# Optimization experiments

Measured on AMD Instinct MI355X. Metric: run time of the kernel, lower is better.

Reference implementation:

```python
import jax, jax.numpy as jnp
import numpy as np

DIM = 192
HEADS = 6
G = 16          # window size (ds_flag=0 dense attention)
B = 1
H_SZ = 256
W_SZ = 256
POS_DIM = 12    # (dim//4)//4
HIDDEN = 768    # 4*dim


def _ln(x, g, b, eps=1e-5):
    m = jnp.mean(x, -1, keepdims=True)
    v = jnp.var(x, -1, keepdims=True)
    return (x - m) / jnp.sqrt(v + eps) * g + b


def setup_inputs() -> dict:
    key = jax.random.key(0)
    ks = jax.random.split(key, 8)
    s = 0.05
    return {
        "x": jax.random.normal(ks[0], (B, H_SZ * W_SZ, DIM), jnp.float32),
        "gamma1": jnp.ones((DIM,), jnp.float32),
        "beta1": jnp.zeros((DIM,), jnp.float32),
        "qkv_w": jax.random.normal(ks[1], (DIM, 3 * DIM), jnp.float32) * s,
        "qkv_b": jnp.zeros((3 * DIM,), jnp.float32),
        "proj_w": jax.random.normal(ks[2], (DIM, DIM), jnp.float32) * s,
        "proj_b": jnp.zeros((DIM,), jnp.float32),
        "pos_proj_w": jax.random.normal(ks[3], (2, POS_DIM), jnp.float32) * s,
        "pos_proj_b": jnp.zeros((POS_DIM,), jnp.float32),
        "ln1_g": jnp.ones((POS_DIM,), jnp.float32),
        "ln1_b": jnp.zeros((POS_DIM,), jnp.float32),
        "pos1_w": jax.random.normal(ks[4], (POS_DIM, POS_DIM), jnp.float32) * s,
        "pos1_b": jnp.zeros((POS_DIM,), jnp.float32),
        "ln2_g": jnp.ones((POS_DIM,), jnp.float32),
        "ln2_b": jnp.zeros((POS_DIM,), jnp.float32),
        "pos2_w": jax.random.normal(ks[5], (POS_DIM, POS_DIM), jnp.float32) * s,
        "pos2_b": jnp.zeros((POS_DIM,), jnp.float32),
        "ln3_g": jnp.ones((POS_DIM,), jnp.float32),
        "ln3_b": jnp.zeros((POS_DIM,), jnp.float32),
        "pos3_w": jax.random.normal(ks[6], (POS_DIM, HEADS), jnp.float32) * s,
        "pos3_b": jnp.zeros((HEADS,), jnp.float32),
        "gamma2": jnp.ones((DIM,), jnp.float32),
        "beta2": jnp.zeros((DIM,), jnp.float32),
        "fc1_w": jax.random.normal(ks[7], (DIM, HIDDEN), jnp.float32) * s,
        "fc1_b": jnp.zeros((HIDDEN,), jnp.float32),
        "fc2_w": jax.random.normal(jax.random.fold_in(key, 9), (HIDDEN, DIM), jnp.float32) * s,
        "fc2_b": jnp.zeros((DIM,), jnp.float32),
        "H": H_SZ,
        "W": W_SZ,
    }


def reference(x, gamma1, beta1, qkv_w, qkv_b, proj_w, proj_b,
              pos_proj_w, pos_proj_b, ln1_g, ln1_b, pos1_w, pos1_b,
              ln2_g, ln2_b, pos2_w, pos2_b, ln3_g, ln3_b, pos3_w, pos3_b,
              gamma2, beta2, fc1_w, fc1_b, fc2_w, fc2_b, H, W):
    Bx, L, C = x.shape
    h = HEADS
    d = C // h
    N = G * G
    shortcut = x
    xn = _ln(x, gamma1, beta1)
    # window partition (H, W divisible by G -> no padding, attn_mask=None)
    xw = xn.reshape(Bx, H // G, G, W // G, G, C).transpose(0, 1, 3, 2, 4, 5)
    xw = xw.reshape(-1, N, C)                       # [B_, N, C]
    B_ = xw.shape[0]
    qkv = (xw @ qkv_w + qkv_b).reshape(B_, N, 3, h, d)
    q = qkv[:, :, 0].transpose(0, 2, 1, 3) * (d ** -0.5)   # [B_, h, N, d]
    k = qkv[:, :, 1].transpose(0, 2, 1, 3)
    v = qkv[:, :, 2].transpose(0, 2, 1, 3)
    attn = jnp.einsum('bhnd,bhmd->bhnm', q, k)      # [B_, h, N, N]
    # dynamic relative position bias (DynamicPosBias MLP + gather)
    r = jnp.arange(1 - G, G)
    biases = jnp.stack(jnp.meshgrid(r, r, indexing='ij')).reshape(2, -1).T.astype(x.dtype)  # [(2G-1)^2, 2]
    p = biases @ pos_proj_w + pos_proj_b
    p = jax.nn.relu(_ln(p, ln1_g, ln1_b)) @ pos1_w + pos1_b
    p = jax.nn.relu(_ln(p, ln2_g, ln2_b)) @ pos2_w + pos2_b
    p = jax.nn.relu(_ln(p, ln3_g, ln3_b)) @ pos3_w + pos3_b  # [(2G-1)^2, heads]
    c = jnp.stack(jnp.meshgrid(jnp.arange(G), jnp.arange(G), indexing='ij')).reshape(2, -1)
    rel = c[:, :, None] - c[:, None, :]             # [2, N, N]
    idx = (rel[0] + G - 1) * (2 * G - 1) + (rel[1] + G - 1)  # [N, N]
    attn = attn + p[idx].transpose(2, 0, 1)[None]   # add [1, h, N, N] bias
    attn = jax.nn.softmax(attn, axis=-1)
    out = jnp.einsum('bhnm,bhmd->bhnd', attn, v).transpose(0, 2, 1, 3).reshape(B_, N, C)
    out = out @ proj_w + proj_b
    # window reverse
    out = out.reshape(Bx, H // G, W // G, G, G, C).transpose(0, 1, 3, 2, 4, 5).reshape(Bx, L, C)
    x = shortcut + out
    y = _ln(x, gamma2, beta2)
    y = jax.nn.gelu(y @ fc1_w + fc1_b, approximate=False) @ fc2_w + fc2_b
    return x + y
```

## Files before the change

### kernel.cpp

```cpp
#include <hip/hip_runtime.h>
#include <hip/hip_bf16.h>

#define DIM 192
#define HEADS 6
#define QKV_N 576
#define HIDDEN 768
#define M_ROWS 65536

typedef unsigned short ushortT;
typedef __attribute__((ext_vector_type(8))) short short8v;
typedef __attribute__((ext_vector_type(4))) float f32x4;
typedef __attribute__((ext_vector_type(4))) unsigned int u32x4;

#define QSCALE_L2E 0.2550348649f
#define LOG2E 1.4426950408889634f

__device__ __forceinline__ float bf2f(ushortT u) {
    union { unsigned int i; float f; } c; c.i = ((unsigned int)u) << 16; return c.f;
}
__device__ __forceinline__ ushortT f2bf(float f) {
    union { float f; unsigned int i; } c; c.f = f;
    unsigned int i = c.i;
    return (ushortT)((i + 0x7fffu + ((i >> 16) & 1u)) >> 16);
}

#define GLOBAL_LOAD_LDS16(gp, lp) \
    __builtin_amdgcn_global_load_lds((const __attribute__((address_space(1))) void*)(gp), \
                                     (__attribute__((address_space(3))) void*)(lp), 16, 0, 0)

__device__ __forceinline__ void ln_relu_mm12(const float* in, const float* g, const float* b,
                                             const float* w, const float* bb, float* out, int nout) {
    float m = 0.f;
#pragma unroll
    for (int j = 0; j < 12; ++j) m += in[j];
    m *= (1.0f / 12.0f);
    float v = 0.f;
#pragma unroll
    for (int j = 0; j < 12; ++j) { float d = in[j] - m; v += d * d; }
    v *= (1.0f / 12.0f);
    float r = rsqrtf(v + 1e-5f);
    float t[12];
#pragma unroll
    for (int j = 0; j < 12; ++j) t[j] = fmaxf((in[j] - m) * r * g[j] + b[j], 0.0f);
    for (int j2 = 0; j2 < nout; ++j2) {
        float s = bb[j2];
#pragma unroll
        for (int j = 0; j < 12; ++j) s = fmaf(t[j], w[j * nout + j2], s);
        out[j2] = s;
    }
}

__global__ __launch_bounds__(256) void prep_kernel(
        const float* __restrict__ qkv_w, const float* __restrict__ proj_w,
        const float* __restrict__ fc1_w, const float* __restrict__ fc2_w,
        ushortT* __restrict__ qkv_wt, ushortT* __restrict__ proj_wt,
        ushortT* __restrict__ fc1_wt, ushortT* __restrict__ fc2_wt,
        const float* __restrict__ pw, const float* __restrict__ pb,
        const float* __restrict__ g1, const float* __restrict__ b1,
        const float* __restrict__ w1, const float* __restrict__ bb1,
        const float* __restrict__ g2, const float* __restrict__ b2,
        const float* __restrict__ w2, const float* __restrict__ bb2,
        const float* __restrict__ g3, const float* __restrict__ b3,
        const float* __restrict__ w3, const float* __restrict__ bb3,
        float* __restrict__ BTf) {
    __shared__ float tile[32][33];
    int blk = blockIdx.x;
    int t = threadIdx.x;
    if (blk < 432) {
        const float* W; ushortT* Wt; int K, N, bx, by;
        if (blk < 108)      { W = qkv_w;  Wt = qkv_wt;  K = 192; N = 576; bx = blk % 18;        by = blk / 18; }
        else if (blk < 144) { int r = blk - 108; W = proj_w; Wt = proj_wt; K = 192; N = 192; bx = r % 6;  by = r / 6; }
        else if (blk < 288) { int r = blk - 144; W = fc1_w;  Wt = fc1_wt;  K = 192; N = 768; bx = r % 24; by = r / 24; }
        else                { int r = blk - 288; W = fc2_w;  Wt = fc2_wt;  K = 768; N = 192; bx = r % 6;  by = r / 6; }
        int tx = t & 31, ty = t >> 5;
        int bX = bx * 32, bY = by * 32;
#pragma unroll
        for (int i = 0; i < 32; i += 8)
            tile[ty + i][tx] = W[(size_t)(bY + ty + i) * N + bX + tx];
        __syncthreads();
#pragma unroll
        for (int i = 0; i < 32; i += 8)
            Wt[(size_t)(bX + ty + i) * K + bY + tx] = f2bf(tile[tx][ty + i]);
    } else {
        int blk2 = blk - 432;
        int h = blk2 >> 8, q = blk2 & 255, kv = t;
        float di = (float)((q >> 4) - (kv >> 4));
        float dj = (float)((q & 15) - (kv & 15));
        float a[12], hh[12];
#pragma unroll
        for (int j = 0; j < 12; ++j) a[j] = di * pw[j] + dj * pw[12 + j] + pb[j];
        ln_relu_mm12(a, g1, b1, w1, bb1, hh, 12);
        ln_relu_mm12(hh, g2, b2, w2, bb2, a, 12);
        float m = 0.f;
#pragma unroll
        for (int j = 0; j < 12; ++j) m += a[j];
        m *= (1.0f / 12.0f);
        float v = 0.f;
#pragma unroll
        for (int j = 0; j < 12; ++j) { float d = a[j] - m; v += d * d; }
        v *= (1.0f / 12.0f);
        float r = rsqrtf(v + 1e-5f);
        float s = bb3[h];
#pragma unroll
        for (int j = 0; j < 12; ++j)
            s = fmaf(fmaxf((a[j] - m) * r * g3[j] + b3[j], 0.0f), w3[j * 6 + h], s);
        int wid = q >> 6, mf = (q >> 4) & 3, l4 = (q >> 2) & 3, rr = q & 3;
        int kc = kv >> 5, cc = kv & 31;
        int cf = (cc >> 4) & 1, l15 = cc & 15;
        int lane = l4 * 16 + l15;
        size_t off = ((size_t)((h * 8 + kc) * 32 + wid * 8 + mf * 2 + cf)) * 256 + lane * 4 + rr;
        BTf[off] = s * LOG2E;
    }
}

__global__ __launch_bounds__(256) void ln_kernel(const float* __restrict__ x,
                                                 const float* __restrict__ g,
                                                 const float* __restrict__ b,
                                                 ushortT* __restrict__ out) {
    int lane = threadIdx.x & 63;
    size_t row = (size_t)blockIdx.x * 4 + (threadIdx.x >> 6);
    const float* xr = x + row * DIM;
    float v0 = xr[lane], v1 = xr[lane + 64], v2 = xr[lane + 128];
    float s = v0 + v1 + v2;
    float ss = v0 * v0 + v1 * v1 + v2 * v2;
#pragma unroll
    for (int off = 32; off > 0; off >>= 1) {
        s += __shfl_xor(s, off);
        ss += __shfl_xor(ss, off);
    }
    float mean = s * (1.0f / DIM);
    float rstd = rsqrtf(ss * (1.0f / DIM) - mean * mean + 1e-5f);
    ushortT* o = out + row * DIM;
    o[lane]       = f2bf((v0 - mean) * rstd * g[lane]       + b[lane]);
    o[lane + 64]  = f2bf((v1 - mean) * rstd * g[lane + 64]  + b[lane + 64]);
    o[lane + 128] = f2bf((v2 - mean) * rstd * g[lane + 128] + b[lane + 128]);
}

template <int MODE, int NY, int KK>
__global__ __launch_bounds__(256) void mfma_gemm(const ushortT* __restrict__ A,
                                                 const ushortT* __restrict__ Wt,
                                                 const float* __restrict__ bias,
                                                 const float* __restrict__ resid,
                                                 void* __restrict__ outp,
                                                 int N) {
    __shared__ ushortT As[2][128 * 64];
    __shared__ ushortT Bs[2][64 * 64];
    const int NT = KK / 64;
    int tid = threadIdx.x;
    int lane = tid & 63, wid = tid >> 6;
    int l15 = lane & 15, l4 = lane >> 4;
    int wr = wid >> 1, wc = wid & 1;
    int p = blockIdx.x;
    int cpx = gridDim.x >> 3;
    int logical = (p & 7) * cpx + (p >> 3);
    int bx = logical / NY;
    int by = logical - bx * NY;
    int bm = bx * 128, bn = by * 64;

    f32x4 acc[4][2];
#pragma unroll
    for (int mf = 0; mf < 4; ++mf)
#pragma unroll
        for (int nf = 0; nf < 2; ++nf)
#pragma unroll
            for (int r = 0; r < 4; ++r) acc[mf][nf][r] = 0.f;

    int srow = tid >> 3;
    int schunk = (tid & 7) ^ (srow & 7);
    const ushortT* agp = A + (size_t)(bm + srow) * KK + schunk * 8;
    const ushortT* bgp = Wt + (size_t)(bn + srow) * KK + schunk * 8;

    auto STAGE = [&](int buf, int t) {
        int k0 = t * 64;
#pragma unroll
        for (int i = 0; i < 4; ++i)
            GLOBAL_LOAD_LDS16(agp + (size_t)i * 32 * KK + k0, &As[buf][i * 2048 + wid * 512]);
#pragma unroll
        for (int i = 0; i < 2; ++i)
            GLOBAL_LOAD_LDS16(bgp + (size_t)i * 32 * KK + k0, &Bs[buf][i * 2048 + wid * 512]);
    };

    STAGE(0, 0);
    for (int t = 0; t < NT; ++t) {
        int cur = t & 1;
        if (t + 1 < NT) {
            STAGE(cur ^ 1, t + 1);
            asm volatile("s_waitcnt vmcnt(6)" ::: "memory");
        } else {
            asm volatile("s_waitcnt vmcnt(0)" ::: "memory");
        }
        __builtin_amdgcn_s_barrier();
        const ushortT* Asc = As[cur];
        const ushortT* Bsc = Bs[cur];
#pragma unroll
        for (int ks = 0; ks < 2; ++ks) {
            short8v af[4], bf[2];
#pragma unroll
            for (int mf = 0; mf < 4; ++mf) {
                int row = wr * 64 + mf * 16 + l15;
                af[mf] = *(const short8v*)&Asc[row * 64 + (((ks * 4 + l4) ^ (l15 & 7)) << 3)];
            }
#pragma unroll
            for (int nf = 0; nf < 2; ++nf) {
                int row = wc * 32 + nf * 16 + l15;
                bf[nf] = *(const short8v*)&Bsc[row * 64 + (((ks * 4 + l4) ^ (l15 & 7)) << 3)];
            }
#pragma unroll
            for (int mf = 0; mf < 4; ++mf)
#pragma unroll
                for (int nf = 0; nf < 2; ++nf)
                    acc[mf][nf] = __builtin_amdgcn_mfma_f32_16x16x32_bf16(af[mf], bf[nf], acc[mf][nf], 0, 0, 0);
        }
        __builtin_amdgcn_s_barrier();
    }
#pragma unroll
    for (int mf = 0; mf < 4; ++mf) {
        size_t row = (size_t)bm + wr * 64 + mf * 16 + l4 * 4;
#pragma unroll
        for (int nf = 0; nf < 2; ++nf) {
            int col = bn + wc * 32 + nf * 16 + l15;
            float bv = bias[col];
#pragma unroll
            for (int r = 0; r < 4; ++r) {
                size_t off = (row + r) * (size_t)N + col;
                float v = acc[mf][nf][r] + bv;
                if (MODE == 0) {
                    if (col < 192) v *= QSCALE_L2E;
                    ((ushortT*)outp)[off] = f2bf(v);
                } else if (MODE == 1) {
                    float x3 = v * v * v;
                    float z = fmaf(x3, -0.1029537917f, v * -2.302205077f);
                    float e = exp2f(z);
                    v = v * __builtin_amdgcn_rcpf(1.0f + e);
                    ((ushortT*)outp)[off] = f2bf(v);
                } else if (MODE == 2) {
                    ((float*)outp)[off] = resid[off] + v;
                } else {
                    ((float*)outp)[off] += v;
                }
            }
        }
    }
}

__global__ __launch_bounds__(256) void attn_mfma_kernel(const ushortT* __restrict__ qkv,
                                                        const float* __restrict__ BTf,
                                                        ushortT* __restrict__ O) {
    __shared__ ushortT Vt[32][264];
    __shared__ unsigned int Ps[4][64][20];
    int wh = blockIdx.x;
    int w = wh / 6, h = wh - w * 6;
    int wi = w >> 4, wj = w & 15;
    int tid = threadIdx.x, lane = tid & 63, wid = tid >> 6;
    int l15 = lane & 15, l4 = lane >> 4;

    {
        int t = tid;
        int pcol = (t & ~31) | (((t & 15) << 1) | ((t >> 4) & 1));
        size_t gr = (size_t)((wi * 16 + (t >> 4)) * 256 + wj * 16 + (t & 15));
        const ushortT* vp = qkv + gr * 576 + 384 + h * 32;
#pragma unroll
        for (int d0 = 0; d0 < 32; d0 += 8) {
            short8v u = *(const short8v*)(vp + d0);
#pragma unroll
            for (int j = 0; j < 8; ++j) Vt[d0 + j][pcol] = (ushortT)u[j];
        }
    }
    short8v qf[4];
    int qbase = wid * 64;
#pragma unroll
    for (int mf = 0; mf < 4; ++mf) {
        int q = qbase + mf * 16 + l15;
        size_t gr = (size_t)((wi * 16 + (q >> 4)) * 256 + wj * 16 + (q & 15));
        qf[mf] = *(const short8v*)(qkv + gr * 576 + h * 32 + l4 * 8);
    }
    __syncthreads();

    float l_run[4][4];
    f32x4 accO[4][2];
#pragma unroll
    for (int mf = 0; mf < 4; ++mf)
#pragma unroll
        for (int r = 0; r < 4; ++r) {
            l_run[mf][r] = 0.f;
            accO[mf][0][r] = 0.f;
            accO[mf][1][r] = 0.f;
        }
    const float* btb = BTf + ((size_t)(h * 8) * 32 + wid * 8) * 256 + lane * 4;

    auto load_kf = [&](int kc, short8v* kf) {
#pragma unroll
        for (int cf = 0; cf < 2; ++cf) {
            int kv = kc * 32 + cf * 16 + l15;
            size_t gr = (size_t)((wi * 16 + (kv >> 4)) * 256 + wj * 16 + (kv & 15));
            kf[cf] = *(const short8v*)(qkv + gr * 576 + 192 + h * 32 + l4 * 8);
        }
    };

    f32x4 bias_buf[8];
    auto load_bias = [&](int kc) {
#pragma unroll
        for (int i = 0; i < 8; ++i)
            bias_buf[i] = *(const f32x4*)(btb + (size_t)(kc * 32 + i) * 256);
    };

    short8v kfA[2], kfB[2];
    load_kf(0, kfA);
    load_bias(0);

    for (int kc = 0; kc < 8; ++kc) {
        if (kc < 7) load_kf(kc + 1, kfB);
        f32x4 s[4][2];
        __builtin_amdgcn_s_setprio(1);
#pragma unroll
        for (int mf = 0; mf < 4; ++mf)
#pragma unroll
            for (int cf = 0; cf < 2; ++cf)
                s[mf][cf] = __builtin_amdgcn_mfma_f32_16x16x32_bf16(qf[mf], kfA[cf], bias_buf[mf * 2 + cf], 0, 0, 0);
        __builtin_amdgcn_s_setprio(0);
        if (kc < 7) load_bias(kc + 1);
#pragma unroll
        for (int mf = 0; mf < 4; ++mf) {
#pragma unroll
            for (int r = 0; r < 4; ++r) {
                float p0 = exp2f(s[mf][0][r]);
                float p1 = exp2f(s[mf][1][r]);
                l_run[mf][r] += p0 + p1;
                unsigned int pk;
                asm("v_cvt_pk_bf16_f32 %0, %1, %2" : "=v"(pk) : "v"(p0), "v"(p1));
                Ps[wid][mf * 16 + 4 * l4 + r][l15] = pk;
            }
        }
        short8v vb[2];
#pragma unroll
        for (int nf = 0; nf < 2; ++nf)
            vb[nf] = *(const short8v*)&Vt[nf * 16 + l15][kc * 32 + l4 * 8];
        __builtin_amdgcn_s_setprio(1);
#pragma unroll
        for (int mf = 0; mf < 4; ++mf) {
            u32x4 pr = *(const u32x4*)&Ps[wid][mf * 16 + l15][l4 * 4];
            short8v pa = __builtin_bit_cast(short8v, pr);
#pragma unroll
            for (int nf = 0; nf < 2; ++nf)
                accO[mf][nf] = __builtin_amdgcn_mfma_f32_16x16x32_bf16(pa, vb[nf], accO[mf][nf], 0, 0, 0);
        }
        __builtin_amdgcn_s_setprio(0);
        kfA[0] = kfB[0]; kfA[1] = kfB[1];
    }
#pragma unroll
    for (int mf = 0; mf < 4; ++mf)
#pragma unroll
        for (int r = 0; r < 4; ++r) {
            float l = l_run[mf][r];
            l += __shfl_xor(l, 1);
            l += __shfl_xor(l, 2);
            l += __shfl_xor(l, 4);
            l += __shfl_xor(l, 8);
            l_run[mf][r] = 1.0f / l;
        }
#pragma unroll
    for (int mf = 0; mf < 4; ++mf) {
        int q0 = qbase + mf * 16 + 4 * l4;
#pragma unroll
        for (int r = 0; r < 4; ++r) {
            int q = q0 + r;
            size_t gr = (size_t)((wi * 16 + (q >> 4)) * 256 + wj * 16 + (q & 15));
            ushortT* op = O + gr * 192 + h * 32 + l15;
            float inv = l_run[mf][r];
            op[0]  = f2bf(accO[mf][0][r] * inv);
            op[16] = f2bf(accO[mf][1][r] * inv);
        }
    }
}

extern "C" void kernel_launch(void* const* d_in, const int* in_sizes, int n_in,
                              void* d_out, int out_size, void* d_ws, size_t ws_size,
                              hipStream_t stream) {
    const float* x        = (const float*)d_in[0];
    const float* gamma1   = (const float*)d_in[1];
    const float* beta1    = (const float*)d_in[2];
    const float* qkv_w    = (const float*)d_in[3];
    const float* qkv_b    = (const float*)d_in[4];
    const float* proj_w   = (const float*)d_in[5];
    const float* proj_b   = (const float*)d_in[6];
    const float* pos_proj_w = (const float*)d_in[7];
    const float* pos_proj_b = (const float*)d_in[8];
    const float* ln1_g    = (const float*)d_in[9];
    const float* ln1_b    = (const float*)d_in[10];
    const float* pos1_w   = (const float*)d_in[11];
    const float* pos1_b   = (const float*)d_in[12];
    const float* ln2_g    = (const float*)d_in[13];
    const float* ln2_b    = (const float*)d_in[14];
    const float* pos2_w   = (const float*)d_in[15];
    const float* pos2_b   = (const float*)d_in[16];
    const float* ln3_g    = (const float*)d_in[17];
    const float* ln3_b    = (const float*)d_in[18];
    const float* pos3_w   = (const float*)d_in[19];
    const float* pos3_b   = (const float*)d_in[20];
    const float* gamma2   = (const float*)d_in[21];
    const float* beta2    = (const float*)d_in[22];
    const float* fc1_w    = (const float*)d_in[23];
    const float* fc1_b    = (const float*)d_in[24];
    const float* fc2_w    = (const float*)d_in[25];
    const float* fc2_b    = (const float*)d_in[26];
    float* out = (float*)d_out;

    char* ws = (char*)d_ws;
    ushortT* qkv = (ushortT*)(ws + 0);
    ushortT* y1  = (ushortT*)(ws + 0);
    ushortT* xn   = (ushortT*)(ws + 100663296);
    ushortT* Obuf = xn;
    ushortT* xn2  = xn;
    ushortT* qkv_wt  = (ushortT*)(ws + 125829120);
    ushortT* proj_wt = (ushortT*)(ws + 126050304);
    ushortT* fc1_wt  = (ushortT*)(ws + 126124032);
    ushortT* fc2_wt  = (ushortT*)(ws + 126418944);
    float*   BTf     = (float*)(ws + 126713856);

    prep_kernel<<<1968, 256, 0, stream>>>(
        qkv_w, proj_w, fc1_w, fc2_w, qkv_wt, proj_wt, fc1_wt, fc2_wt,
        pos_proj_w, pos_proj_b, ln1_g, ln1_b, pos1_w, pos1_b,
        ln2_g, ln2_b, pos2_w, pos2_b, ln3_g, ln3_b, pos3_w, pos3_b, BTf);
    ln_kernel<<<M_ROWS / 4, 256, 0, stream>>>(x, gamma1, beta1, xn);
    mfma_gemm<0, 9, 192><<<(M_ROWS / 128) * (QKV_N / 64), 256, 0, stream>>>(
        xn, qkv_wt, qkv_b, nullptr, qkv, QKV_N);
    attn_mfma_kernel<<<1536, 256, 0, stream>>>(qkv, BTf, Obuf);
    mfma_gemm<2, 3, 192><<<(M_ROWS / 128) * (DIM / 64), 256, 0, stream>>>(
        Obuf, proj_wt, proj_b, x, out, DIM);
    ln_kernel<<<M_ROWS / 4, 256, 0, stream>>>(out, gamma2, beta2, xn2);
    mfma_gemm<1, 12, 192><<<(M_ROWS / 128) * (HIDDEN / 64), 256, 0, stream>>>(
        xn2, fc1_wt, fc1_b, nullptr, y1, HIDDEN);
    mfma_gemm<3, 3, 768><<<(M_ROWS / 128) * (DIM / 64), 256, 0, stream>>>(
        y1, fc2_wt, fc2_b, nullptr, out, DIM);
}
```

Baseline: 232.6 us.

## Drop K/bias register prefetch and interleave per-fragment QK, softmax, PV for occupancy

```diff
diff --git a/kernel.cpp b/kernel.cpp
--- a/kernel.cpp
+++ b/kernel.cpp
@@ -243,9 +243,9 @@
     }
 }
 
-__global__ __launch_bounds__(256) void attn_mfma_kernel(const ushortT* __restrict__ qkv,
-                                                        const float* __restrict__ BTf,
-                                                        ushortT* __restrict__ O) {
+__global__ __launch_bounds__(256, 4) void attn_mfma_kernel(const ushortT* __restrict__ qkv,
+                                                           const float* __restrict__ BTf,
+                                                           ushortT* __restrict__ O) {
     __shared__ ushortT Vt[32][264];
     __shared__ unsigned int Ps[4][64][20];
     int wh = blockIdx.x;
@@ -288,64 +288,42 @@
         }
     const float* btb = BTf + ((size_t)(h * 8) * 32 + wid * 8) * 256 + lane * 4;
 
-    auto load_kf = [&](int kc, short8v* kf) {
+    for (int kc = 0; kc < 8; ++kc) {
+        short8v kf[2];
 #pragma unroll
         for (int cf = 0; cf < 2; ++cf) {
             int kv = kc * 32 + cf * 16 + l15;
             size_t gr = (size_t)((wi * 16 + (kv >> 4)) * 256 + wj * 16 + (kv & 15));
             kf[cf] = *(const short8v*)(qkv + gr * 576 + 192 + h * 32 + l4 * 8);
         }
-    };
-
-    f32x4 bias_buf[8];
-    auto load_bias = [&](int kc) {
-#pragma unroll
-        for (int i = 0; i < 8; ++i)
-            bias_buf[i] = *(const f32x4*)(btb + (size_t)(kc * 32 + i) * 256);
-    };
-
-    short8v kfA[2], kfB[2];
-    load_kf(0, kfA);
-    load_bias(0);
-
-    for (int kc = 0; kc < 8; ++kc) {
-        if (kc < 7) load_kf(kc + 1, kfB);
-        f32x4 s[4][2];
-        __builtin_amdgcn_s_setprio(1);
-#pragma unroll
-        for (int mf = 0; mf < 4; ++mf)
-#pragma unroll
-            for (int cf = 0; cf < 2; ++cf)
-                s[mf][cf] = __builtin_amdgcn_mfma_f32_16x16x32_bf16(qf[mf], kfA[cf], bias_buf[mf * 2 + cf], 0, 0, 0);
-        __builtin_amdgcn_s_setprio(0);
-        if (kc < 7) load_bias(kc + 1);
+        short8v vb[2];
+#pragma unroll
+        for (int nf = 0; nf < 2; ++nf)
+            vb[nf] = *(const short8v*)&Vt[nf * 16 + l15][kc * 32 + l4 * 8];
 #pragma unroll
         for (int mf = 0; mf < 4; ++mf) {
+            f32x4 s0 = *(const f32x4*)(btb + (size_t)(kc * 32 + mf * 2 + 0) * 256);
+            f32x4 s1 = *(const f32x4*)(btb + (size_t)(kc * 32 + mf * 2 + 1) * 256);
+            __builtin_amdgcn_s_setprio(1);
+            s0 = __builtin_amdgcn_mfma_f32_16x16x32_bf16(qf[mf], kf[0], s0, 0, 0, 0);
+            s1 = __builtin_amdgcn_mfma_f32_16x16x32_bf16(qf[mf], kf[1], s1, 0, 0, 0);
+            __builtin_amdgcn_s_setprio(0);
 #pragma unroll
             for (int r = 0; r < 4; ++r) {
-                float p0 = exp2f(s[mf][0][r]);
-                float p1 = exp2f(s[mf][1][r]);
+                float p0 = exp2f(s0[r]);
+                float p1 = exp2f(s1[r]);
                 l_run[mf][r] += p0 + p1;
                 unsigned int pk;
                 asm("v_cvt_pk_bf16_f32 %0, %1, %2" : "=v"(pk) : "v"(p0), "v"(p1));
                 Ps[wid][mf * 16 + 4 * l4 + r][l15] = pk;
             }
-        }
-        short8v vb[2];
-#pragma unroll
-        for (int nf = 0; nf < 2; ++nf)
-            vb[nf] = *(const short8v*)&Vt[nf * 16 + l15][kc * 32 + l4 * 8];
-        __builtin_amdgcn_s_setprio(1);
-#pragma unroll
-        for (int mf = 0; mf < 4; ++mf) {
             u32x4 pr = *(const u32x4*)&Ps[wid][mf * 16 + l15][l4 * 4];
             short8v pa = __builtin_bit_cast(short8v, pr);
-#pragma unroll
-            for (int nf = 0; nf < 2; ++nf)
-                accO[mf][nf] = __builtin_amdgcn_mfma_f32_16x16x32_bf16(pa, vb[nf], accO[mf][nf], 0, 0, 0);
-        }
-        __builtin_amdgcn_s_setprio(0);
-        kfA[0] = kfB[0]; kfA[1] = kfB[1];
+            __builtin_amdgcn_s_setprio(1);
+            accO[mf][0] = __builtin_amdgcn_mfma_f32_16x16x32_bf16(pa, vb[0], accO[mf][0], 0, 0, 0);
+            accO[mf][1] = __builtin_amdgcn_mfma_f32_16x16x32_bf16(pa, vb[1], accO[mf][1], 0, 0, 0);
+            __builtin_amdgcn_s_setprio(0);
+        }
     }
 #pragma unroll
     for (int mf = 0; mf < 4; ++mf)
```

Measured after the change: 230.5 us. Within noise of the previous version (-0.9%).
